# Performance work log

Measured on AMD Instinct MI355X. Metric: run time of the kernel, lower is better.

Reference implementation:

```python
import jax, jax.numpy as jnp
import numpy as np

K_HOPS = 10
ALPHA = 0.1
N_NODES = 50000
N_EDGES = 600000
F_IN = 128
HIDDEN = 64
N_CLASSES = 40


def setup_inputs() -> dict:
    key = jax.random.key(0)
    k1, k2, k3, k4 = jax.random.split(key, 4)
    x = jax.random.normal(k1, (N_NODES, F_IN), dtype=jnp.float32)
    edge_index = jax.random.randint(k2, (2, N_EDGES), 0, N_NODES, dtype=jnp.int32)
    edge_weight = jnp.ones((N_EDGES,), dtype=jnp.float32)
    W1 = jax.random.normal(k3, (F_IN, HIDDEN), dtype=jnp.float32) * (1.0 / np.sqrt(F_IN))
    b1 = jnp.zeros((HIDDEN,), dtype=jnp.float32)
    W2 = jax.random.normal(k4, (HIDDEN, N_CLASSES), dtype=jnp.float32) * (1.0 / np.sqrt(HIDDEN))
    b2 = jnp.zeros((N_CLASSES,), dtype=jnp.float32)
    return {"x": x, "edge_index": edge_index, "edge_weight": edge_weight,
            "W1": W1, "b1": b1, "W2": W2, "b2": b2}


def reference(x, edge_index, edge_weight, W1, b1, W2, b2):
    n = x.shape[0]
    # GCN symmetric normalization with self-loops (tfg gcn cache)
    self_idx = jnp.arange(n, dtype=edge_index.dtype)
    row = jnp.concatenate([edge_index[0], self_idx])
    col = jnp.concatenate([edge_index[1], self_idx])
    w = jnp.concatenate([edge_weight, jnp.ones((n,), dtype=edge_weight.dtype)])
    deg = jax.ops.segment_sum(w, row, num_segments=n)
    dinv = jnp.where(deg > 0, jax.lax.rsqrt(jnp.maximum(deg, 1e-12)), 0.0)
    nw = dinv[row] * w * dinv[col]  # [E+N] normalized edge weights

    def prop(h):
        # h_out[i] = sum_{(i,j)} nw * h[j]
        return jax.ops.segment_sum(h[col] * nw[:, None], row, num_segments=n)

    def step(h, _):
        h_next = prop(h)
        return h_next, None

    # SSGC: out = (1-alpha)/K * sum_{l=1..K} T^l x + alpha * x
    def step_acc(carry, _):
        h, acc = carry
        h_next = prop(h)
        return (h_next, acc + h_next), None

    (_, acc), _ = jax.lax.scan(step_acc, (x, jnp.zeros_like(x)), None, length=K_HOPS)
    h = (1.0 - ALPHA) / K_HOPS * acc + ALPHA * x  # [N, F]

    h = jax.nn.relu(h @ W1 + b1)  # [N, HIDDEN]
    logits = h @ W2 + b2          # [N, N_CLASSES]
    return logits
```

## Files before the change

kernel.cpp:

```cpp
#include <hip/hip_runtime.h>
#include <hip/hip_fp16.h>
#include <math.h>

constexpr int   N   = 50000;
constexpr int   E   = 600000;
constexpr int   FIN = 128;
constexpr int   H   = 64;
constexpr int   C   = 40;
constexpr int   K   = 10;
constexpr float CK  = (1.0f - 0.1f) / 10.0f;
constexpr float AL  = 0.1f;

typedef float v2f __attribute__((ext_vector_type(2)));

__device__ __forceinline__ unsigned pack_fp8x4(float f0, float f1, float f2, float f3) {
    unsigned r = __builtin_amdgcn_cvt_pk_fp8_f32(f0, f1, 0u, false);
    r = __builtin_amdgcn_cvt_pk_fp8_f32(f2, f3, r, true);
    return r;
}

__device__ __forceinline__ float ep_w(unsigned v) {
    return __half2float(__ushort_as_half((unsigned short)(v >> 16)));
}
__device__ __forceinline__ unsigned ep_pack(int c, float w) {
    return (unsigned)(unsigned short)c |
           ((unsigned)__half_as_ushort(__float2half_rn(w)) << 16);
}

constexpr int G1N  = 64;
constexpr int XPAD = 132;
__global__ __launch_bounds__(256, 2) void k_gemm1(const float* __restrict__ x,
                                                  const float* __restrict__ W1,
                                                  float* __restrict__ y0,
                                                  unsigned char* __restrict__ y0f8) {
    __shared__ float ws[FIN * H];
    __shared__ float xs[G1N * XPAD];
    const float4* W14 = (const float4*)W1;
    const float4* x4  = (const float4*)x;
    int t = threadIdx.x;
    int node0 = blockIdx.x * G1N;
    for (int i = t; i < FIN * H / 4; i += 256) ((float4*)ws)[i] = W14[i];
    for (int p = 0; p < 8; ++p) {
        int idx = p * 256 + t;
        int n   = idx >> 5;
        int kk  = idx & 31;
        int node = node0 + n;
        float4 v = (node < N) ? x4[(size_t)node * (FIN / 4) + kk]
                              : make_float4(0.f, 0.f, 0.f, 0.f);
        *(float4*)(xs + n * XPAD + kk * 4) = v;
    }
    __syncthreads();
    int nb = (t >> 4) * 4;
    int cb = (t & 15) * 4;
    float a00=0,a01=0,a02=0,a03=0, a10=0,a11=0,a12=0,a13=0;
    float a20=0,a21=0,a22=0,a23=0, a30=0,a31=0,a32=0,a33=0;
#pragma unroll 8
    for (int k = 0; k < FIN; ++k) {
        float4 wv = *(const float4*)(ws + k * H + cb);
        float x0 = xs[(nb + 0) * XPAD + k];
        float x1 = xs[(nb + 1) * XPAD + k];
        float x2 = xs[(nb + 2) * XPAD + k];
        float x3 = xs[(nb + 3) * XPAD + k];
        a00 = fmaf(x0, wv.x, a00); a01 = fmaf(x0, wv.y, a01);
        a02 = fmaf(x0, wv.z, a02); a03 = fmaf(x0, wv.w, a03);
        a10 = fmaf(x1, wv.x, a10); a11 = fmaf(x1, wv.y, a11);
        a12 = fmaf(x1, wv.z, a12); a13 = fmaf(x1, wv.w, a13);
        a20 = fmaf(x2, wv.x, a20); a21 = fmaf(x2, wv.y, a21);
        a22 = fmaf(x2, wv.z, a22); a23 = fmaf(x2, wv.w, a23);
        a30 = fmaf(x3, wv.x, a30); a31 = fmaf(x3, wv.y, a31);
        a32 = fmaf(x3, wv.z, a32); a33 = fmaf(x3, wv.w, a33);
    }
    float4 rows[4] = {make_float4(a00,a01,a02,a03), make_float4(a10,a11,a12,a13),
                      make_float4(a20,a21,a22,a23), make_float4(a30,a31,a32,a33)};
#pragma unroll
    for (int i = 0; i < 4; ++i) {
        int node = node0 + nb + i;
        if (node >= N) break;
        float4 r = rows[i];
        *(float4*)(y0 + (size_t)node * H + cb) = r;
        *(unsigned*)(y0f8 + (size_t)node * H + cb) = pack_fp8x4(r.x, r.y, r.z, r.w);
    }
}

__global__ void k_count(const int* __restrict__ row, int* __restrict__ cnt8) {
    int e = blockIdx.x * blockDim.x + threadIdx.x;
    if (e >= E) return;
    atomicAdd(&cnt8[(size_t)(blockIdx.x & 7) * N + row[e]], 1);
}

__global__ __launch_bounds__(1024) void k_scan_blocks(const int* __restrict__ cnt8,
                                                      int* __restrict__ row_ptr,
                                                      int* __restrict__ bsum) {
    __shared__ int s[1024];
    int gid = blockIdx.x * 1024 + threadIdx.x;
    int v = 0;
    if (gid < N) {
#pragma unroll
        for (int c = 0; c < 8; ++c) v += cnt8[(size_t)c * N + gid];
    }
    s[threadIdx.x] = v;
    __syncthreads();
    for (int off = 1; off < 1024; off <<= 1) {
        int t = (threadIdx.x >= off) ? s[threadIdx.x - off] : 0;
        __syncthreads();
        s[threadIdx.x] += t;
        __syncthreads();
    }
    if (gid < N) row_ptr[gid] = s[threadIdx.x] - v;
    if (threadIdx.x == 1023) bsum[blockIdx.x] = s[1023];
}

__global__ void k_scan_sums(const int* __restrict__ bsum, int* __restrict__ boff, int nb) {
    int lane = threadIdx.x;
    int orig = (lane < nb) ? bsum[lane] : 0;
    int v = orig;
    for (int off = 1; off < 64; off <<= 1) {
        int t = __shfl_up(v, off, 64);
        if (lane >= off) v += t;
    }
    if (lane < nb) boff[lane] = v - orig;
}

__global__ __launch_bounds__(1024) void k_addoff(int* __restrict__ row_ptr,
                                                 const int* __restrict__ boff,
                                                 int* __restrict__ cnt8) {
    int gid = blockIdx.x * 1024 + threadIdx.x;
    if (gid < N) {
        int rp = row_ptr[gid] + boff[blockIdx.x];
        row_ptr[gid] = rp;
        int off = rp;
#pragma unroll
        for (int c = 0; c < 8; ++c) {
            int t = cnt8[(size_t)c * N + gid];
            cnt8[(size_t)c * N + gid] = off;
            off += t;
        }
    }
    if (gid == 0) row_ptr[N] = E;
}

__global__ void k_scatter(const int* __restrict__ row, const int* __restrict__ col,
                          const float* __restrict__ w,
                          int* __restrict__ off8, unsigned* __restrict__ ep) {
    int e = blockIdx.x * blockDim.x + threadIdx.x;
    if (e >= E) return;
    int r = row[e];
    int p = atomicAdd(&off8[(size_t)(blockIdx.x & 7) * N + r], 1);
    ep[p] = ep_pack(col[e], w[e]);
}

__global__ void k_deg_dinv(const unsigned* __restrict__ ep, const int* __restrict__ row_ptr,
                           float* __restrict__ dinv, float* __restrict__ dinv2) {
    int i = blockIdx.x * blockDim.x + threadIdx.x;
    if (i >= N) return;
    float d = 1.0f;
    int e0 = row_ptr[i], e1 = row_ptr[i + 1];
    for (int j = e0; j < e1; ++j) d += ep_w(ep[j]);
    float di = rsqrtf(d);
    dinv[i]  = di;
    dinv2[i] = di * di;
}

__global__ __launch_bounds__(256) void k_norm(unsigned* __restrict__ ep,
                                              const int* __restrict__ row_ptr,
                                              const float* __restrict__ dinv) {
    int node = blockIdx.x * 32 + (threadIdx.x >> 3);
    if (node >= N) return;
    int l = threadIdx.x & 7;
    float dr = dinv[node];
    int e0 = row_ptr[node], e1 = row_ptr[node + 1];
    for (int j = e0 + l; j < e1; j += 8) {
        unsigned v = ep[j];
        int c = v & 0xFFFFu;
        ep[j] = ep_pack(c, ep_w(v) * dr * dinv[c]);
    }
}

constexpr int HSP = 68;
template <bool WRITE_H, bool ACC_INIT, bool FINAL>
__global__ __launch_bounds__(256) void k_prop(const uint2* __restrict__ hin,
                                              uint2* __restrict__ hout,
                                              __half* __restrict__ acch,
                                              const float* __restrict__ dinv2,
                                              const int* __restrict__ row_ptr,
                                              const unsigned* __restrict__ ep,
                                              const float4* __restrict__ y04,
                                              const float* __restrict__ b1,
                                              const float* __restrict__ W2,
                                              const float* __restrict__ b2,
                                              float* __restrict__ out) {
    extern __shared__ float smem[];
    float* w2s = smem;
    float* hs  = smem + H * C;
    float* b2s = hs + 32 * HSP;
    float* b1s = b2s + C;
    int t = threadIdx.x;
    if (FINAL) {
        for (int i = t; i < H * C; i += 256) w2s[i] = W2[i];
        if (t < C) b2s[t] = b2[t];
        if (t < H) b1s[t] = b1[t];
        __syncthreads();
    }
    int lane = t & 63;
    int nib  = (t >> 6) * 8 + (lane >> 3);
    int l    = lane & 7;
    int node = blockIdx.x * 32 + nib;
    bool nv  = node < N;
    int nodec = nv ? node : N - 1;
    int start = row_ptr[nodec];
    int deg   = nv ? (row_ptr[nodec + 1] - start) : 0;
    int md = deg;
#pragma unroll
    for (int off = 8; off <= 32; off <<= 1) md = max(md, __shfl_xor(md, off, 64));
    float s[8];
#pragma unroll
    for (int i = 0; i < 8; ++i) s[i] = 0.f;
    auto accum = [&](uint2 v, float w) {
        v2f p0 = __builtin_amdgcn_cvt_pk_f32_fp8(v.x, false);
        v2f p1 = __builtin_amdgcn_cvt_pk_f32_fp8(v.x, true);
        v2f p2 = __builtin_amdgcn_cvt_pk_f32_fp8(v.y, false);
        v2f p3 = __builtin_amdgcn_cvt_pk_f32_fp8(v.y, true);
        s[0] = fmaf(w, p0.x, s[0]); s[1] = fmaf(w, p0.y, s[1]);
        s[2] = fmaf(w, p1.x, s[2]); s[3] = fmaf(w, p1.y, s[3]);
        s[4] = fmaf(w, p2.x, s[4]); s[5] = fmaf(w, p2.y, s[5]);
        s[6] = fmaf(w, p3.x, s[6]); s[7] = fmaf(w, p3.y, s[7]);
    };
    for (int j = 0; j < md; j += 2) {
        bool a0 = j < deg, a1 = j + 1 < deg;
        unsigned e0 = ep[a0 ? start + j     : 0];
        unsigned e1 = ep[a1 ? start + j + 1 : 0];
        uint2 v0 = hin[(size_t)(e0 & 0xFFFFu) * 8 + l];
        uint2 v1 = hin[(size_t)(e1 & 0xFFFFu) * 8 + l];
        float w0 = a0 ? ep_w(e0) : 0.0f;
        float w1 = a1 ? ep_w(e1) : 0.0f;
        accum(v0, w0);
        accum(v1, w1);
    }
    if (nv) {
        size_t base = (size_t)nodec * 8 + l;
        accum(hin[base], dinv2[nodec]);
        if (WRITE_H) {
            uint2 o;
            o.x = pack_fp8x4(s[0], s[1], s[2], s[3]);
            o.y = pack_fp8x4(s[4], s[5], s[6], s[7]);
            hout[base] = o;
        }
        uint4* ap = (uint4*)(acch + (size_t)nodec * H + l * 8);
        if (FINAL) {
            uint4 old = *ap;
            const unsigned* u = (const unsigned*)&old;
#pragma unroll
            for (int d = 0; d < 4; ++d) {
                float2 f = __half22float2(*(__half2*)&u[d]);
                s[2*d+0] += f.x; s[2*d+1] += f.y;
            }
            float4 ya = y04[(size_t)nodec * (H / 4) + 2 * l];
            float4 yb = y04[(size_t)nodec * (H / 4) + 2 * l + 1];
            const float* bp = b1s + l * 8;
            float* hp = hs + nib * HSP + l * 8;
            hp[0] = fmaxf(fmaf(CK, s[0], fmaf(AL, ya.x, bp[0])), 0.f);
            hp[1] = fmaxf(fmaf(CK, s[1], fmaf(AL, ya.y, bp[1])), 0.f);
            hp[2] = fmaxf(fmaf(CK, s[2], fmaf(AL, ya.z, bp[2])), 0.f);
            hp[3] = fmaxf(fmaf(CK, s[3], fmaf(AL, ya.w, bp[3])), 0.f);
            hp[4] = fmaxf(fmaf(CK, s[4], fmaf(AL, yb.x, bp[4])), 0.f);
            hp[5] = fmaxf(fmaf(CK, s[5], fmaf(AL, yb.y, bp[5])), 0.f);
            hp[6] = fmaxf(fmaf(CK, s[6], fmaf(AL, yb.z, bp[6])), 0.f);
            hp[7] = fmaxf(fmaf(CK, s[7], fmaf(AL, yb.w, bp[7])), 0.f);
        } else {
            if (!ACC_INIT) {
                uint4 old = *ap;
                const unsigned* u = (const unsigned*)&old;
#pragma unroll
                for (int d = 0; d < 4; ++d) {
                    float2 f = __half22float2(*(__half2*)&u[d]);
                    s[2*d+0] += f.x; s[2*d+1] += f.y;
                }
            }
            uint4 nvp;
            unsigned* u = (unsigned*)&nvp;
#pragma unroll
            for (int d = 0; d < 4; ++d) {
                __half2 h = __floats2half2_rn(s[2*d+0], s[2*d+1]);
                u[d] = *(unsigned*)&h;
            }
            *ap = nvp;
        }
    }
    if (FINAL) {
        __syncthreads();
        int node0 = blockIdx.x * 32;
        for (int o = t; o < 32 * C; o += 256) {
            int nl = o / C, c = o % C;
            int n2 = node0 + nl;
            if (n2 >= N) continue;
            float v = b2s[c];
            const float* hr = &hs[nl * HSP];
#pragma unroll
            for (int k = 0; k < H; ++k) v = fmaf(hr[k], w2s[k * C + c], v);
            out[n2 * C + c] = v;
        }
    }
}

extern "C" void kernel_launch(void* const* d_in, const int* in_sizes, int n_in,
                              void* d_out, int out_size, void* d_ws, size_t ws_size,
                              hipStream_t stream) {
    const float* x  = (const float*)d_in[0];
    const int*   ei = (const int*)d_in[1];
    const float* ew = (const float*)d_in[2];
    const float* W1 = (const float*)d_in[3];
    const float* b1 = (const float*)d_in[4];
    const float* W2 = (const float*)d_in[5];
    const float* b2 = (const float*)d_in[6];
    float* out = (float*)d_out;

    const int* row = ei;
    const int* col = ei + E;

    char* ws = (char*)d_ws;
    size_t off = 0;
    auto alloc = [&](size_t bytes) -> char* {
        char* p = ws + off;
        off = (off + bytes + 1023) & ~(size_t)1023;
        return p;
    };
    float*         y0   = (float*)alloc((size_t)N * H * 4);
    unsigned char* y0f8 = (unsigned char*)alloc((size_t)N * H);
    unsigned char* ha   = (unsigned char*)alloc((size_t)N * H);
    unsigned char* hb   = (unsigned char*)alloc((size_t)N * H);
    __half*        acch = (__half*)alloc((size_t)N * H * 2);
    int*      cnt8   = (int*)     alloc((size_t)8 * N * 4);
    float*    dinv   = (float*)   alloc((size_t)N * 4);
    float*    dinv2  = (float*)   alloc((size_t)N * 4);
    int*      row_ptr= (int*)     alloc((size_t)(N + 1) * 4);
    int*      bsum   = (int*)     alloc(64 * 4);
    int*      boff   = (int*)     alloc(64 * 4);
    unsigned* ep     = (unsigned*)alloc((size_t)E * 4);

    hipMemsetAsync(cnt8, 0, (size_t)8 * N * 4, stream);

    k_gemm1<<<(N + G1N - 1) / G1N, 256, 0, stream>>>(x, W1, y0, y0f8);

    k_count<<<(E + 255) / 256, 256, 0, stream>>>(row, cnt8);

    constexpr int NB = (N + 1023) / 1024;
    k_scan_blocks<<<NB, 1024, 0, stream>>>(cnt8, row_ptr, bsum);
    k_scan_sums<<<1, 64, 0, stream>>>(bsum, boff, NB);
    k_addoff<<<NB, 1024, 0, stream>>>(row_ptr, boff, cnt8);

    k_scatter<<<(E + 255) / 256, 256, 0, stream>>>(row, col, ew, cnt8, ep);
    k_deg_dinv<<<(N + 255) / 256, 256, 0, stream>>>(ep, row_ptr, dinv, dinv2);
    k_norm<<<(N + 31) / 32, 256, 0, stream>>>(ep, row_ptr, dinv);

    const uint2* hin = (const uint2*)y0f8;
    uint2* bufs[2] = {(uint2*)ha, (uint2*)hb};
    const float4* y04 = (const float4*)y0;
    int grid = (N + 31) / 32;
    size_t smemF = (size_t)(H * C + 32 * HSP + C + H) * 4;
    for (int hop = 0; hop < K; ++hop) {
        uint2* hout = bufs[hop & 1];
        if (hop == 0)
            k_prop<true, true, false><<<grid, 256, 0, stream>>>(hin, hout, acch, dinv2,
                row_ptr, ep, y04, b1, W2, b2, out);
        else if (hop == K - 1)
            k_prop<false, false, true><<<grid, 256, smemF, stream>>>(hin, hout, acch, dinv2,
                row_ptr, ep, y04, b1, W2, b2, out);
        else
            k_prop<true, false, false><<<grid, 256, 0, stream>>>(hin, hout, acch, dinv2,
                row_ptr, ep, y04, b1, W2, b2, out);
        hin = hout;
    }
}
```

Baseline: 334.3 us.

## Fuse all propagation hops into one persistent cooperative kernel with grid sync

Replaces the ten per-hop propagation launches with a single cooperative kernel. Each block owns two 32-node tiles and keeps the hop accumulator in registers across hops, separated by grid-wide syncs. The final ReLU MLP epilogue runs in the same kernel. This removes the launch overhead and the fp16 accumulator read/write traffic on every hop. The edge loop is also unrolled to four gathers per iteration. The trade-offs are the cost of each grid barrier and the need for every block to be co-resident, with a fallback to the old multi-launch path if the cooperative launch fails.

```diff
diff --git a/kernel.cpp b/kernel.cpp
--- a/kernel.cpp
+++ b/kernel.cpp
@@ -1,6 +1,9 @@
 #include <hip/hip_runtime.h>
 #include <hip/hip_fp16.h>
+#include <hip/hip_cooperative_groups.h>
 #include <math.h>
+
+namespace cg = cooperative_groups;
 
 constexpr int   N   = 50000;
 constexpr int   E   = 600000;
@@ -25,6 +28,17 @@
 __device__ __forceinline__ unsigned ep_pack(int c, float w) {
     return (unsigned)(unsigned short)c |
            ((unsigned)__half_as_ushort(__float2half_rn(w)) << 16);
+}
+
+__device__ __forceinline__ void accum8(float* s, uint2 v, float w) {
+    v2f p0 = __builtin_amdgcn_cvt_pk_f32_fp8(v.x, false);
+    v2f p1 = __builtin_amdgcn_cvt_pk_f32_fp8(v.x, true);
+    v2f p2 = __builtin_amdgcn_cvt_pk_f32_fp8(v.y, false);
+    v2f p3 = __builtin_amdgcn_cvt_pk_f32_fp8(v.y, true);
+    s[0] = fmaf(w, p0.x, s[0]); s[1] = fmaf(w, p0.y, s[1]);
+    s[2] = fmaf(w, p1.x, s[2]); s[3] = fmaf(w, p1.y, s[3]);
+    s[4] = fmaf(w, p2.x, s[4]); s[5] = fmaf(w, p2.y, s[5]);
+    s[6] = fmaf(w, p3.x, s[6]); s[7] = fmaf(w, p3.y, s[7]);
 }
 
 constexpr int G1N  = 64;
@@ -176,7 +190,137 @@
     }
 }
 
-constexpr int HSP = 68;
+constexpr int HSP   = 68;
+constexpr int NTILE = (N + 31) / 32;
+constexpr int NBLK  = (NTILE + 1) / 2;
+
+__global__ __launch_bounds__(256, 4) void k_hops(
+        const uint2* __restrict__ h0,
+        uint2* __restrict__ ha, uint2* __restrict__ hb,
+        const float* __restrict__ dinv2,
+        const int* __restrict__ row_ptr,
+        const unsigned* __restrict__ ep,
+        const float4* __restrict__ y04,
+        const float* __restrict__ b1,
+        const float* __restrict__ W2,
+        const float* __restrict__ b2,
+        float* __restrict__ out) {
+    __shared__ float w2s[H * C];
+    __shared__ float hs[32 * HSP];
+    __shared__ float b2s[C];
+    __shared__ float b1s[H];
+    cg::grid_group grid = cg::this_grid();
+
+    int t = threadIdx.x;
+    for (int i = t; i < H * C; i += 256) w2s[i] = W2[i];
+    if (t < C) b2s[t] = b2[t];
+    if (t < H) b1s[t] = b1[t];
+
+    int lane = t & 63;
+    int nib  = (t >> 6) * 8 + (lane >> 3);
+    int l    = lane & 7;
+
+    int tile0 = blockIdx.x * 2;
+
+    int   ndc[2], start[2], deg[2], md[2], selfb[2];
+    bool  nv[2];
+    float d2[2];
+#pragma unroll
+    for (int ti = 0; ti < 2; ++ti) {
+        int tile = tile0 + ti;
+        int nd   = tile * 32 + nib;
+        nv[ti]   = (tile < NTILE) && (nd < N);
+        int nc   = nv[ti] ? nd : N - 1;
+        ndc[ti]  = nc;
+        start[ti] = row_ptr[nc];
+        deg[ti]   = nv[ti] ? (row_ptr[nc + 1] - start[ti]) : 0;
+        int m = deg[ti];
+#pragma unroll
+        for (int off = 8; off <= 32; off <<= 1) m = max(m, __shfl_xor(m, off, 64));
+        md[ti]    = m;
+        d2[ti]    = dinv2[nc];
+        selfb[ti] = nc * 8 + l;
+    }
+
+    float acc[2][8];
+#pragma unroll
+    for (int ti = 0; ti < 2; ++ti)
+#pragma unroll
+        for (int i = 0; i < 8; ++i) acc[ti][i] = 0.f;
+
+    const uint2* hi = h0;
+    for (int hop = 0; hop < K; ++hop) {
+        uint2* ho = (hop & 1) ? hb : ha;
+        bool last = (hop == K - 1);
+#pragma unroll
+        for (int ti = 0; ti < 2; ++ti) {
+            float s[8];
+#pragma unroll
+            for (int i = 0; i < 8; ++i) s[i] = 0.f;
+            int st = start[ti], dg = deg[ti];
+            for (int j = 0; j < md[ti]; j += 4) {
+                bool a0 = j < dg, a1 = j + 1 < dg, a2 = j + 2 < dg, a3 = j + 3 < dg;
+                unsigned e0 = ep[a0 ? st + j     : 0];
+                unsigned e1 = ep[a1 ? st + j + 1 : 0];
+                unsigned e2 = ep[a2 ? st + j + 2 : 0];
+                unsigned e3 = ep[a3 ? st + j + 3 : 0];
+                uint2 v0 = hi[(size_t)(e0 & 0xFFFFu) * 8 + l];
+                uint2 v1 = hi[(size_t)(e1 & 0xFFFFu) * 8 + l];
+                uint2 v2 = hi[(size_t)(e2 & 0xFFFFu) * 8 + l];
+                uint2 v3 = hi[(size_t)(e3 & 0xFFFFu) * 8 + l];
+                accum8(s, v0, a0 ? ep_w(e0) : 0.f);
+                accum8(s, v1, a1 ? ep_w(e1) : 0.f);
+                accum8(s, v2, a2 ? ep_w(e2) : 0.f);
+                accum8(s, v3, a3 ? ep_w(e3) : 0.f);
+            }
+            if (nv[ti]) {
+                accum8(s, hi[selfb[ti]], d2[ti]);
+#pragma unroll
+                for (int i = 0; i < 8; ++i) acc[ti][i] += s[i];
+                if (!last) {
+                    uint2 o;
+                    o.x = pack_fp8x4(s[0], s[1], s[2], s[3]);
+                    o.y = pack_fp8x4(s[4], s[5], s[6], s[7]);
+                    ho[selfb[ti]] = o;
+                }
+            }
+        }
+        if (!last) grid.sync();
+        hi = ho;
+    }
+
+#pragma unroll
+    for (int ti = 0; ti < 2; ++ti) {
+        __syncthreads();
+        if (nv[ti]) {
+            float4 ya = y04[(size_t)ndc[ti] * (H / 4) + 2 * l];
+            float4 yb = y04[(size_t)ndc[ti] * (H / 4) + 2 * l + 1];
+            const float* bp = b1s + l * 8;
+            float* hp = hs + nib * HSP + l * 8;
+            hp[0] = fmaxf(fmaf(CK, acc[ti][0], fmaf(AL, ya.x, bp[0])), 0.f);
+            hp[1] = fmaxf(fmaf(CK, acc[ti][1], fmaf(AL, ya.y, bp[1])), 0.f);
+            hp[2] = fmaxf(fmaf(CK, acc[ti][2], fmaf(AL, ya.z, bp[2])), 0.f);
+            hp[3] = fmaxf(fmaf(CK, acc[ti][3], fmaf(AL, ya.w, bp[3])), 0.f);
+            hp[4] = fmaxf(fmaf(CK, acc[ti][4], fmaf(AL, yb.x, bp[4])), 0.f);
+            hp[5] = fmaxf(fmaf(CK, acc[ti][5], fmaf(AL, yb.y, bp[5])), 0.f);
+            hp[6] = fmaxf(fmaf(CK, acc[ti][6], fmaf(AL, yb.z, bp[6])), 0.f);
+            hp[7] = fmaxf(fmaf(CK, acc[ti][7], fmaf(AL, yb.w, bp[7])), 0.f);
+        }
+        __syncthreads();
+        int node0 = (tile0 + ti) * 32;
+        for (int o = t; o < 32 * C; o += 256) {
+            int nl = o / C, c = o % C;
+            int n2 = node0 + nl;
+            if (n2 >= N) continue;
+            float v = b2s[c];
+            const float* hr = &hs[nl * HSP];
+#pragma unroll
+            for (int k = 0; k < H; ++k) v = fmaf(hr[k], w2s[k * C + c], v);
+            out[n2 * C + c] = v;
+        }
+    }
+}
+
 template <bool WRITE_H, bool ACC_INIT, bool FINAL>
 __global__ __launch_bounds__(256) void k_prop(const uint2* __restrict__ hin,
                                               uint2* __restrict__ hout,
@@ -215,30 +359,18 @@
     float s[8];
 #pragma unroll
     for (int i = 0; i < 8; ++i) s[i] = 0.f;
-    auto accum = [&](uint2 v, float w) {
-        v2f p0 = __builtin_amdgcn_cvt_pk_f32_fp8(v.x, false);
-        v2f p1 = __builtin_amdgcn_cvt_pk_f32_fp8(v.x, true);
-        v2f p2 = __builtin_amdgcn_cvt_pk_f32_fp8(v.y, false);
-        v2f p3 = __builtin_amdgcn_cvt_pk_f32_fp8(v.y, true);
-        s[0] = fmaf(w, p0.x, s[0]); s[1] = fmaf(w, p0.y, s[1]);
-        s[2] = fmaf(w, p1.x, s[2]); s[3] = fmaf(w, p1.y, s[3]);
-        s[4] = fmaf(w, p2.x, s[4]); s[5] = fmaf(w, p2.y, s[5]);
-        s[6] = fmaf(w, p3.x, s[6]); s[7] = fmaf(w, p3.y, s[7]);
-    };
     for (int j = 0; j < md; j += 2) {
         bool a0 = j < deg, a1 = j + 1 < deg;
         unsigned e0 = ep[a0 ? start + j     : 0];
         unsigned e1 = ep[a1 ? start + j + 1 : 0];
         uint2 v0 = hin[(size_t)(e0 & 0xFFFFu) * 8 + l];
         uint2 v1 = hin[(size_t)(e1 & 0xFFFFu) * 8 + l];
-        float w0 = a0 ? ep_w(e0) : 0.0f;
-        float w1 = a1 ? ep_w(e1) : 0.0f;
-        accum(v0, w0);
-        accum(v1, w1);
+        accum8(s, v0, a0 ? ep_w(e0) : 0.0f);
+        accum8(s, v1, a1 ? ep_w(e1) : 0.0f);
     }
     if (nv) {
         size_t base = (size_t)nodec * 8 + l;
-        accum(hin[base], dinv2[nodec]);
+        accum8(s, hin[base], dinv2[nodec]);
         if (WRITE_H) {
             uint2 o;
             o.x = pack_fp8x4(s[0], s[1], s[2], s[3]);
@@ -352,22 +484,34 @@
     k_deg_dinv<<<(N + 255) / 256, 256, 0, stream>>>(ep, row_ptr, dinv, dinv2);
     k_norm<<<(N + 31) / 32, 256, 0, stream>>>(ep, row_ptr, dinv);
 
-    const uint2* hin = (const uint2*)y0f8;
-    uint2* bufs[2] = {(uint2*)ha, (uint2*)hb};
+    const uint2* h0 = (const uint2*)y0f8;
+    uint2* hA = (uint2*)ha;
+    uint2* hB = (uint2*)hb;
     const float4* y04 = (const float4*)y0;
-    int grid = (N + 31) / 32;
-    size_t smemF = (size_t)(H * C + 32 * HSP + C + H) * 4;
-    for (int hop = 0; hop < K; ++hop) {
-        uint2* hout = bufs[hop & 1];
-        if (hop == 0)
-            k_prop<true, true, false><<<grid, 256, 0, stream>>>(hin, hout, acch, dinv2,
-                row_ptr, ep, y04, b1, W2, b2, out);
-        else if (hop == K - 1)
-            k_prop<false, false, true><<<grid, 256, smemF, stream>>>(hin, hout, acch, dinv2,
-                row_ptr, ep, y04, b1, W2, b2, out);
-        else
-            k_prop<true, false, false><<<grid, 256, 0, stream>>>(hin, hout, acch, dinv2,
-                row_ptr, ep, y04, b1, W2, b2, out);
-        hin = hout;
-    }
-}
+    void* kargs[] = {(void*)&h0, (void*)&hA, (void*)&hB, (void*)&dinv2,
+                     (void*)&row_ptr, (void*)&ep, (void*)&y04,
+                     (void*)&b1, (void*)&W2, (void*)&b2, (void*)&out};
+    hipError_t cerr = hipLaunchCooperativeKernel((const void*)k_hops,
+                                                 dim3(NBLK), dim3(256),
+                                                 kargs, 0, stream);
+    if (cerr != hipSuccess) {
+        (void)hipGetLastError();
+        const uint2* hin = (const uint2*)y0f8;
+        uint2* bufs[2] = {(uint2*)ha, (uint2*)hb};
+        int grid = (N + 31) / 32;
+        size_t smemF = (size_t)(H * C + 32 * HSP + C + H) * 4;
+        for (int hop = 0; hop < K; ++hop) {
+            uint2* hout = bufs[hop & 1];
+            if (hop == 0)
+                k_prop<true, true, false><<<grid, 256, 0, stream>>>(hin, hout, acch, dinv2,
+                    row_ptr, ep, y04, b1, W2, b2, out);
+            else if (hop == K - 1)
+                k_prop<false, false, true><<<grid, 256, smemF, stream>>>(hin, hout, acch, dinv2,
+                    row_ptr, ep, y04, b1, W2, b2, out);
+            else
+                k_prop<true, false, false><<<grid, 256, 0, stream>>>(hin, hout, acch, dinv2,
+                    row_ptr, ep, y04, b1, W2, b2, out);
+            hin = hout;
+        }
+    }
+}
```

After: 1.139 ms. 3.41x slower.
